# Performance work log

Hardware: AMD Instinct MI355X
Metric: run time of the kernel (lower is better)

The kernel has to match this reference:

```python
import jax, jax.numpy as jnp
import numpy as np

VOCAB = 20000
TOP_K = 8
GLOVE = 300
OUT_C = 100
B, L, N_LABELS = 32, 128, 8


def setup_inputs() -> dict:
    key = jax.random.key(0)
    k1, k2, k3, k4 = jax.random.split(key, 4)
    detect_labels = jax.random.randint(k1, (B, L, N_LABELS), 0, VOCAB, dtype=jnp.int32)
    # knowledge_fact_dict materialized as a dense table: [vocab, top_k, 600]
    fact_table = jax.random.normal(k2, (VOCAB, TOP_K, 2 * GLOVE), dtype=jnp.float32)
    # 1x1 Conv2d(300 -> 100) == linear map over channel dim
    conv_w = jax.random.normal(k3, (OUT_C, GLOVE), dtype=jnp.float32) * (1.0 / np.sqrt(GLOVE))
    conv_b = jax.random.normal(k4, (OUT_C,), dtype=jnp.float32) * 0.01
    return {"detect_labels": detect_labels, "fact_table": fact_table,
            "conv_w": conv_w, "conv_b": conv_b}


def reference(detect_labels, fact_table, conv_w, conv_b):
    b, l, n_labels = detect_labels.shape
    k = fact_table.shape[1]
    # vectorized gather replacing the per-label Python dict lookup
    facts = fact_table[detect_labels.reshape(-1)]            # [N, K, 600]
    facts = facts.reshape(-1, 2 * k, GLOVE)                  # [N, 2K, 300]
    # 1x1 conv over channel dim 300 -> 100
    y = jnp.einsum('nkc,oc->nko', facts, conv_w) + conv_b    # [N, 2K, 100]
    y = y.reshape(b * l, n_labels * 2 * k, OUT_C)            # [B*L, n_labels*2K, 100]
    y = y.mean(axis=1).reshape(b, l, OUT_C)                  # [B, L, 100]
    return y  # dropout is identity at eval
```

## Files before the change

kernel.cpp:

```cpp
#include <hip/hip_runtime.h>

#define VOCAB   20000
#define GLOVE   300
#define C4      75
#define RTOT    16
#define OUTC    100
#define NLAB    8
#define NOUT    4096
#define FT_ROW  (RTOT * GLOVE)
#define ROWS_A  16
#define NITEM   (ROWS_A * C4)

__global__ __launch_bounds__(256) void k_flags(const int* __restrict__ labels,
                                               int* __restrict__ flags, int n) {
    int i = blockIdx.x * 256 + threadIdx.x;
    if (i < n) flags[labels[i]] = 1;
}

__global__ __launch_bounds__(256) void k_reduce_proj(const float* __restrict__ ft,
                                                     const float* __restrict__ W,
                                                     const int* __restrict__ flags,
                                                     float* __restrict__ proj) {
    __shared__ float lds[ROWS_A * GLOVE];
    const int vbase = blockIdx.x * ROWS_A;
    const int tid = threadIdx.x;

    for (int i = tid; i < NITEM; i += 256) {
        const int r  = i / C4;
        const int cg = i - r * C4;
        const int v  = vbase + r;
        float sx = 0.f, sy = 0.f, sz = 0.f, sw = 0.f;
        if (flags[v]) {
            const float4* p = reinterpret_cast<const float4*>(
                ft + (size_t)v * FT_ROW + (size_t)cg * 4);
            #pragma unroll
            for (int k = 0; k < RTOT; ++k) {
                float4 t = p[k * C4];
                sx += t.x; sy += t.y; sz += t.z; sw += t.w;
            }
        }
        reinterpret_cast<float4*>(lds)[i] = make_float4(sx, sy, sz, sw);
    }
    __syncthreads();

    const int wave = tid >> 6;
    const int lane = tid & 63;
    const int r0 = wave * 4;
    const int o0 = lane;
    const int o1 = lane + 64;
    const int o1c = (o1 < OUTC) ? o1 : (OUTC - 1);

    float acc0[4] = {0.f, 0.f, 0.f, 0.f};
    float acc1[4] = {0.f, 0.f, 0.f, 0.f};
    const float4* W0 = reinterpret_cast<const float4*>(W + (size_t)o0  * GLOVE);
    const float4* W1 = reinterpret_cast<const float4*>(W + (size_t)o1c * GLOVE);
    const float4* L4 = reinterpret_cast<const float4*>(lds);

    for (int c = 0; c < C4; ++c) {
        const float4 w0 = W0[c];
        const float4 w1 = W1[c];
        #pragma unroll
        for (int i = 0; i < 4; ++i) {
            const float4 s = L4[(r0 + i) * C4 + c];
            acc0[i] += s.x * w0.x + s.y * w0.y + s.z * w0.z + s.w * w0.w;
            acc1[i] += s.x * w1.x + s.y * w1.y + s.z * w1.z + s.w * w1.w;
        }
    }
    #pragma unroll
    for (int i = 0; i < 4; ++i) {
        const size_t v = (size_t)(vbase + r0 + i);
        proj[v * OUTC + o0] = acc0[i];
        if (o1 < OUTC) proj[v * OUTC + o1] = acc1[i];
    }
}

__global__ __launch_bounds__(256) void k_gather(const int* __restrict__ labels,
                                                const float* __restrict__ proj,
                                                const float* __restrict__ bias,
                                                float* __restrict__ out) {
    const int idx = blockIdx.x * 256 + threadIdx.x;
    if (idx >= NOUT * OUTC) return;
    const int n = idx / OUTC;
    const int o = idx - n * OUTC;
    const int* lab = labels + n * NLAB;
    float s = 0.f;
    #pragma unroll
    for (int j = 0; j < NLAB; ++j) {
        s += proj[(size_t)lab[j] * OUTC + o];
    }
    out[idx] = s * (1.0f / 128.0f) + bias[o];
}

__global__ __launch_bounds__(128) void k_direct(const int* __restrict__ labels,
                                                const float* __restrict__ ft,
                                                const float* __restrict__ W,
                                                const float* __restrict__ bias,
                                                float* __restrict__ out) {
    __shared__ float4 sv[C4];
    const int n = blockIdx.x;
    const int tid = threadIdx.x;
    if (tid < C4) {
        float sx = 0.f, sy = 0.f, sz = 0.f, sw = 0.f;
        for (int j = 0; j < NLAB; ++j) {
            const int v = labels[n * NLAB + j];
            const float4* p = reinterpret_cast<const float4*>(
                ft + (size_t)v * FT_ROW + (size_t)tid * 4);
            #pragma unroll
            for (int k = 0; k < RTOT; ++k) {
                float4 t = p[k * C4];
                sx += t.x; sy += t.y; sz += t.z; sw += t.w;
            }
        }
        sv[tid] = make_float4(sx, sy, sz, sw);
    }
    __syncthreads();
    if (tid < OUTC) {
        const float4* w4 = reinterpret_cast<const float4*>(W + (size_t)tid * GLOVE);
        float a = 0.f;
        for (int c = 0; c < C4; ++c) {
            const float4 w = w4[c];
            const float4 s = sv[c];
            a += s.x * w.x + s.y * w.y + s.z * w.z + s.w * w.w;
        }
        out[(size_t)n * OUTC + tid] = a * (1.0f / 128.0f) + bias[tid];
    }
}

extern "C" void kernel_launch(void* const* d_in, const int* in_sizes, int n_in,
                              void* d_out, int out_size, void* d_ws, size_t ws_size,
                              hipStream_t stream) {
    const int*   labels = (const int*)d_in[0];
    const float* ft     = (const float*)d_in[1];
    const float* W      = (const float*)d_in[2];
    const float* bias   = (const float*)d_in[3];
    float* out = (float*)d_out;

    const size_t flags_bytes = (size_t)VOCAB * sizeof(int);
    const size_t proj_bytes  = (size_t)VOCAB * OUTC * sizeof(float);

    if (ws_size >= flags_bytes + proj_bytes) {
        int*   flags = (int*)d_ws;
        float* proj  = (float*)((char*)d_ws + flags_bytes);
        hipMemsetAsync(flags, 0, flags_bytes, stream);
        const int nlabels = NOUT * NLAB;
        k_flags<<<(nlabels + 255) / 256, 256, 0, stream>>>(labels, flags, nlabels);
        k_reduce_proj<<<VOCAB / ROWS_A, 256, 0, stream>>>(ft, W, flags, proj);
        k_gather<<<(NOUT * OUTC + 255) / 256, 256, 0, stream>>>(labels, proj, bias, out);
    } else {
        k_direct<<<NOUT, 128, 0, stream>>>(labels, ft, W, bias, out);
    }
}
```

Measured before the change: 569.5 us.

## Transpose conv weights, use nontemporal fact loads, vectorize gather with float2

Adds a small kernel that transposes the 1x1 conv weights into channel-group-major float4 layout. Lanes in the projection loop then read consecutive output channels, so those loads coalesce instead of striding across rows. Fact-table reads switch to nontemporal vector loads so the large streamed table does not pollute cache. The gather kernel now handles two outputs per thread with float2 accesses. The extra launch and workspace add a little overhead, and the main cost is still reading the table from memory.

```diff
diff --git a/kernel.cpp b/kernel.cpp
--- a/kernel.cpp
+++ b/kernel.cpp
@@ -11,14 +11,25 @@
 #define ROWS_A  16
 #define NITEM   (ROWS_A * C4)
 
+typedef float v4f __attribute__((ext_vector_type(4)));
+
 __global__ __launch_bounds__(256) void k_flags(const int* __restrict__ labels,
                                                int* __restrict__ flags, int n) {
     int i = blockIdx.x * 256 + threadIdx.x;
     if (i < n) flags[labels[i]] = 1;
 }
 
+__global__ __launch_bounds__(256) void k_wt(const float4* __restrict__ W4,
+                                            float4* __restrict__ Wtg) {
+    int i = blockIdx.x * 256 + threadIdx.x;
+    if (i < C4 * OUTC) {
+        int g = i / OUTC, o = i - g * OUTC;
+        Wtg[i] = W4[(size_t)o * C4 + g];
+    }
+}
+
 __global__ __launch_bounds__(256) void k_reduce_proj(const float* __restrict__ ft,
-                                                     const float* __restrict__ W,
+                                                     const float4* __restrict__ Wtg,
                                                      const int* __restrict__ flags,
                                                      float* __restrict__ proj) {
     __shared__ float lds[ROWS_A * GLOVE];
@@ -29,17 +40,17 @@
         const int r  = i / C4;
         const int cg = i - r * C4;
         const int v  = vbase + r;
-        float sx = 0.f, sy = 0.f, sz = 0.f, sw = 0.f;
+        v4f s = {0.f, 0.f, 0.f, 0.f};
         if (flags[v]) {
-            const float4* p = reinterpret_cast<const float4*>(
+            const v4f* p = reinterpret_cast<const v4f*>(
                 ft + (size_t)v * FT_ROW + (size_t)cg * 4);
             #pragma unroll
             for (int k = 0; k < RTOT; ++k) {
-                float4 t = p[k * C4];
-                sx += t.x; sy += t.y; sz += t.z; sw += t.w;
+                v4f t = __builtin_nontemporal_load(p + k * C4);
+                s += t;
             }
         }
-        reinterpret_cast<float4*>(lds)[i] = make_float4(sx, sy, sz, sw);
+        reinterpret_cast<v4f*>(lds)[i] = s;
     }
     __syncthreads();
 
@@ -52,16 +63,14 @@
 
     float acc0[4] = {0.f, 0.f, 0.f, 0.f};
     float acc1[4] = {0.f, 0.f, 0.f, 0.f};
-    const float4* W0 = reinterpret_cast<const float4*>(W + (size_t)o0  * GLOVE);
-    const float4* W1 = reinterpret_cast<const float4*>(W + (size_t)o1c * GLOVE);
-    const float4* L4 = reinterpret_cast<const float4*>(lds);
+    const v4f* L4 = reinterpret_cast<const v4f*>(lds);
 
-    for (int c = 0; c < C4; ++c) {
-        const float4 w0 = W0[c];
-        const float4 w1 = W1[c];
+    for (int g = 0; g < C4; ++g) {
+        const float4 w0 = Wtg[g * OUTC + o0];
+        const float4 w1 = Wtg[g * OUTC + o1c];
         #pragma unroll
         for (int i = 0; i < 4; ++i) {
-            const float4 s = L4[(r0 + i) * C4 + c];
+            const v4f s = L4[(r0 + i) * C4 + g];
             acc0[i] += s.x * w0.x + s.y * w0.y + s.z * w0.z + s.w * w0.w;
             acc1[i] += s.x * w1.x + s.y * w1.y + s.z * w1.z + s.w * w1.w;
         }
@@ -74,21 +83,25 @@
     }
 }
 
+#define OUT2 (OUTC / 2)
 __global__ __launch_bounds__(256) void k_gather(const int* __restrict__ labels,
-                                                const float* __restrict__ proj,
-                                                const float* __restrict__ bias,
-                                                float* __restrict__ out) {
+                                                const float2* __restrict__ proj2,
+                                                const float2* __restrict__ bias2,
+                                                float2* __restrict__ out2) {
     const int idx = blockIdx.x * 256 + threadIdx.x;
-    if (idx >= NOUT * OUTC) return;
-    const int n = idx / OUTC;
-    const int o = idx - n * OUTC;
+    if (idx >= NOUT * OUT2) return;
+    const int n = idx / OUT2;
+    const int o = idx - n * OUT2;
     const int* lab = labels + n * NLAB;
-    float s = 0.f;
+    float sx = 0.f, sy = 0.f;
     #pragma unroll
     for (int j = 0; j < NLAB; ++j) {
-        s += proj[(size_t)lab[j] * OUTC + o];
+        const float2 p = proj2[(size_t)lab[j] * OUT2 + o];
+        sx += p.x; sy += p.y;
     }
-    out[idx] = s * (1.0f / 128.0f) + bias[o];
+    const float2 b = bias2[o];
+    out2[idx] = make_float2(sx * (1.0f / 128.0f) + b.x,
+                            sy * (1.0f / 128.0f) + b.y);
 }
 
 __global__ __launch_bounds__(128) void k_direct(const int* __restrict__ labels,
@@ -136,16 +149,21 @@
     float* out = (float*)d_out;
 
     const size_t flags_bytes = (size_t)VOCAB * sizeof(int);
+    const size_t wt_bytes    = (size_t)C4 * OUTC * sizeof(float4);
     const size_t proj_bytes  = (size_t)VOCAB * OUTC * sizeof(float);
 
-    if (ws_size >= flags_bytes + proj_bytes) {
-        int*   flags = (int*)d_ws;
-        float* proj  = (float*)((char*)d_ws + flags_bytes);
+    if (ws_size >= flags_bytes + wt_bytes + proj_bytes) {
+        int*    flags = (int*)d_ws;
+        float4* Wtg   = (float4*)((char*)d_ws + flags_bytes);
+        float*  proj  = (float*)((char*)d_ws + flags_bytes + wt_bytes);
+
         hipMemsetAsync(flags, 0, flags_bytes, stream);
         const int nlabels = NOUT * NLAB;
         k_flags<<<(nlabels + 255) / 256, 256, 0, stream>>>(labels, flags, nlabels);
-        k_reduce_proj<<<VOCAB / ROWS_A, 256, 0, stream>>>(ft, W, flags, proj);
-        k_gather<<<(NOUT * OUTC + 255) / 256, 256, 0, stream>>>(labels, proj, bias, out);
+        k_wt<<<(C4 * OUTC + 255) / 256, 256, 0, stream>>>((const float4*)W, Wtg);
+        k_reduce_proj<<<VOCAB / ROWS_A, 256, 0, stream>>>(ft, Wtg, flags, proj);
+        k_gather<<<(NOUT * OUT2 + 255) / 256, 256, 0, stream>>>(
+            labels, (const float2*)proj, (const float2*)bias, (float2*)out);
     } else {
         k_direct<<<NOUT, 128, 0, stream>>>(labels, ft, W, bias, out);
     }
```

New measurement: 503.9 us. 1.13x faster.
